# Performance work log

Hardware: AMD Instinct MI355X
Metric: run time of the kernel (lower is better)

## Reference

```python
import jax, jax.numpy as jnp
import numpy as np

GH, GW = 8, 8  # hypernetwork patch grid
EPS = 1e-5


def image_coords(b, h, w, dtype):
    # matches get_image_coordinates: channel0 = x (varies along W), channel1 = y (varies along H)
    xs = jnp.linspace(-1.0, 1.0, w, dtype=dtype)
    ys = jnp.linspace(-1.0, 1.0, h, dtype=dtype)
    X = jnp.broadcast_to(xs[None, :], (h, w))
    Y = jnp.broadcast_to(ys[:, None], (h, w))
    g = jnp.stack([X, Y], axis=0)  # [2,H,W]
    return jnp.broadcast_to(g[None], (b, 2, h, w))


def im2col3(x):
    # reflect-pad 3x3 im2col -> [B,C,9,H,W]
    H, W = x.shape[2], x.shape[3]
    xp = jnp.pad(x, ((0, 0), (0, 0), (1, 1), (1, 1)), mode='reflect')
    cols = [xp[:, :, i:i + H, j:j + W] for i in range(3) for j in range(3)]
    return jnp.stack(cols, axis=2)


def meta_dw3(x, wsig):
    # depthwise 3x3 conv with per-patch weights. wsig: [B, C*9, GH, GW]
    B, C, H, W = x.shape
    p, q = H // GH, W // GW
    cols = im2col3(x).reshape(B, C, 9, GH, p, GW, q)
    Wd = wsig.reshape(B, C, 9, GH, GW)
    out = jnp.einsum('bctuivj,bctuv->bcuivj', cols, Wd)
    return out.reshape(B, C, H, W)


def meta_pw(x, wsig, out_nc):
    # pointwise 1x1 conv with per-patch weights. wsig: [B, out_nc*C, GH, GW]
    B, C, H, W = x.shape
    p, q = H // GH, W // GW
    xr = x.reshape(B, C, GH, p, GW, q)
    Wp = wsig.reshape(B, out_nc, C, GH, GW)
    out = jnp.einsum('bcuivj,bocuv->bouivj', xr, Wp)
    return out.reshape(B, out_nc, H, W)


def batch_norm(x, g, b):
    m = jnp.mean(x, (0, 2, 3), keepdims=True)
    v = jnp.var(x, (0, 2, 3), keepdims=True)
    return (x - m) * jax.lax.rsqrt(v + EPS) * g[None, :, None, None] + b[None, :, None, None]


def relu6(x):
    return jnp.clip(x, 0.0, 6.0)


def hpir(x, wsig, out_nc, g_dw, b_dw, g_pw, b_pw):
    # HyperPatchInvertedResidual, expand_ratio=1, stride=1, in_nc != out_nc -> no residual
    C = x.shape[1]
    n_dw = C * 9
    h = relu6(batch_norm(meta_dw3(x, wsig[:, :n_dw]), g_dw, b_dw))
    h = batch_norm(meta_pw(h, wsig[:, n_dw:n_dw + out_nc * C], out_nc), g_pw, b_pw)
    return h


def resize_bilinear(p, hw):
    B, C = p.shape[0], p.shape[1]
    return jax.image.resize(p, (B, C, hw[0], hw[1]), method='bilinear')


def decoder_forward(x_img, f0, f1, w0, w1, w2,
                    g_dw0, b_dw0, g_pw0, b_pw0,
                    g_dw1, b_dw1, g_pw1, b_pw1,
                    g_dw2, b_dw2, g_pw2, b_pw2):
    feats = [x_img, f0, f1]  # [img] + features[:-1]
    level_w = [w0, w1, w2]
    level_out = [64, 32, 21]
    bn_p = [(g_dw0, b_dw0, g_pw0, b_pw0),
            (g_dw1, b_dw1, g_pw1, b_pw1),
            (g_dw2, b_dw2, g_pw2, b_pw2)]
    p = None
    for level in range(3):
        f = feats[-level - 1]
        if p is None:
            p = f
        else:
            if p.shape[2:] != f.shape[2:]:
                p = resize_bilinear(p, f.shape[2:])
            p = jnp.concatenate([f, p], axis=1)
        B, _, H, W = p.shape
        p = jnp.concatenate([image_coords(B, H, W, p.dtype), p], axis=1)
        g_dw, b_dw, g_pw, b_pw = bn_p[level]
        p = hpir(p, level_w[level], level_out[level], g_dw, b_dw, g_pw, b_pw)
    return p


def setup_inputs() -> dict:
    key = jax.random.key(0)
    ks = jax.random.split(key, 8)
    inp = {
        'x_img': jax.random.normal(ks[0], (4, 3, 256, 256), jnp.float32),
        'f0': jax.random.normal(ks[1], (4, 32, 64, 64), jnp.float32),
        'f1': jax.random.normal(ks[2], (4, 64, 32, 32), jnp.float32),
        'w0': jax.random.normal(ks[3], (4, 4818, 8, 8), jnp.float32) * 0.1,
        'w1': jax.random.normal(ks[4], (4, 4018, 8, 8), jnp.float32) * 0.1,
        'w2': jax.random.normal(ks[5], (4, 1110, 8, 8), jnp.float32) * 0.1,
    }
    for name, c in [('dw0', 66), ('pw0', 64), ('dw1', 98), ('pw1', 32), ('dw2', 37), ('pw2', 21)]:
        inp['g_' + name] = jnp.ones((c,), jnp.float32)
        inp['b_' + name] = jnp.zeros((c,), jnp.float32)
    return inp


def reference(x_img, f0, f1, w0, w1, w2,
              g_dw0, b_dw0, g_pw0, b_pw0,
              g_dw1, b_dw1, g_pw1, b_pw1,
              g_dw2, b_dw2, g_pw2, b_pw2):
    return decoder_forward(x_img, f0, f1, w0, w1, w2,
                           g_dw0, b_dw0, g_pw0, b_pw0,
                           g_dw1, b_dw1, g_pw1, b_pw1,
                           g_dw2, b_dw2, g_pw2, b_pw2)
```

## Files before the change

### kernel.cpp

```cpp
#include <hip/hip_runtime.h>

#define EPS 1e-5f

__device__ __forceinline__ int reflect_idx(int i, int n) {
    if (i < 0) return -i;
    if (i >= n) return 2 * n - 2 - i;
    return i;
}

__device__ __forceinline__ float bilin(const float* __restrict__ pb, int Hp, float sy, float sx) {
    int y0 = (int)floorf(sy), x0 = (int)floorf(sx);
    float fy = sy - y0, fx = sx - x0;
    int y0c = min(max(y0, 0), Hp - 1), y1c = min(max(y0 + 1, 0), Hp - 1);
    int x0c = min(max(x0, 0), Hp - 1), x1c = min(max(x0 + 1, 0), Hp - 1);
    float v00 = pb[y0c * Hp + x0c], v01 = pb[y0c * Hp + x1c];
    float v10 = pb[y1c * Hp + x0c], v11 = pb[y1c * Hp + x1c];
    return v00 * (1 - fy) * (1 - fx) + v01 * (1 - fy) * fx
         + v10 * fy * (1 - fx) + v11 * fy * fx;
}

__device__ __forceinline__ void reduce_ss_lds(const float* __restrict__ part,
                                              const float* __restrict__ g,
                                              const float* __restrict__ bb,
                                              float* ss, int C, float invN, int tid) {
    for (int c = tid; c < C; c += 256) {
        float s1 = 0.f, s2 = 0.f;
#pragma unroll 8
        for (int s = 0; s < 64; ++s) {
            s1 += part[s * 2 * C + 2 * c];
            s2 += part[s * 2 * C + 2 * c + 1];
        }
        float m = s1 * invN;
        float var = s2 * invN - m * m;
        float sc = g[c] * rsqrtf(var + EPS);
        ss[2 * c] = sc;
        ss[2 * c + 1] = bb[c] - m * sc;
    }
}

template <int LEVEL, bool WRITE>
__global__ __launch_bounds__(256)
void fused_dw_kernel(const float* __restrict__ feat, const float* __restrict__ prev,
                     const float* __restrict__ part_prev, const float* __restrict__ g_prev,
                     const float* __restrict__ b_prev, float invN_prev,
                     const float* __restrict__ wsig,
                     float* __restrict__ out, float* __restrict__ part) {
    constexpr int C    = LEVEL == 0 ? 66 : LEVEL == 1 ? 98 : 37;
    constexpr int H    = LEVEL == 0 ? 32 : LEVEL == 1 ? 64 : 256;
    constexpr int TILE = LEVEL == 2 ? 32 : 16;
    constexpr int NT   = H / TILE;
    constexpr int PXPT = (TILE * TILE) / 256;
    constexpr int WC   = LEVEL == 0 ? 4818 : LEVEL == 1 ? 4018 : 1110;
    constexpr int NF   = LEVEL == 0 ? 64 : LEVEL == 1 ? 32 : 3;
    constexpr int Hp   = LEVEL == 1 ? 32 : 64;
    constexpr int Cp   = LEVEL == 1 ? 64 : 32;
    constexpr int P    = H / 8;
    constexpr float SC = LEVEL == 1 ? 0.5f : 0.25f;
    constexpr int HS   = TILE + 2;
    constexpr int PSS  = (LEVEL == 0) ? 2 : 2 * Cp;

    __shared__ float sh[HS * HS];
    __shared__ float pssl[PSS];
    int tid = threadIdx.x, bid = blockIdx.x;
    int tile = bid % (NT * NT);
    int c = (bid / (NT * NT)) % C;
    int b = bid / (NT * NT * C);
    int ty0 = (tile / NT) * TILE, tx0 = (tile % NT) * TILE;

    if constexpr (LEVEL != 0) {
        reduce_ss_lds(part_prev, g_prev, b_prev, pssl, Cp, invN_prev, tid);
        __syncthreads();
    }

    for (int i = tid; i < HS * HS; i += 256) {
        int h = reflect_idx(ty0 - 1 + i / HS, H);
        int w = reflect_idx(tx0 - 1 + i % HS, H);
        float val;
        if (c == 0)      val = -1.f + 2.f * w / (H - 1);
        else if (c == 1) val = -1.f + 2.f * h / (H - 1);
        else if (c < 2 + NF) val = feat[((size_t)(b * NF + c - 2) * H + h) * H + w];
        else {
            int o = c - 2 - NF;
            const float* pb = prev + (size_t)(b * Cp + o) * Hp * Hp;
            float raw = bilin(pb, Hp, (h + 0.5f) * SC - 0.5f, (w + 0.5f) * SC - 0.5f);
            val = raw * pssl[2 * o] + pssl[2 * o + 1];
        }
        sh[i] = val;
    }
    __syncthreads();

    float s1 = 0.f, s2 = 0.f;
    float* ob = out + (((size_t)(b * C + c)) * H + ty0) * H + tx0;
    float wreg[9];
    if constexpr (TILE == P) {
        const float* wb = wsig + ((size_t)(b * WC + c * 9)) * 64 + (ty0 / P) * 8 + (tx0 / P);
#pragma unroll
        for (int t = 0; t < 9; ++t) wreg[t] = wb[(size_t)t * 64];
    }
#pragma unroll
    for (int k = 0; k < PXPT; ++k) {
        int px = tid + k * 256;
        int tyy = px / TILE, txx = px % TILE;
        if constexpr (TILE != P) {
            int u = (ty0 + tyy) / P, vv = (tx0 + txx) / P;
            const float* wb = wsig + ((size_t)(b * WC + c * 9)) * 64 + u * 8 + vv;
#pragma unroll
            for (int t = 0; t < 9; ++t) wreg[t] = wb[(size_t)t * 64];
        }
        float acc = 0.f;
#pragma unroll
        for (int t = 0; t < 9; ++t)
            acc += wreg[t] * sh[(tyy + t / 3) * HS + txx + t % 3];
        if constexpr (WRITE) ob[tyy * H + txx] = acc;
        s1 += acc; s2 += acc * acc;
    }
#pragma unroll
    for (int off = 32; off; off >>= 1) {
        s1 += __shfl_xor(s1, off);
        s2 += __shfl_xor(s2, off);
    }
    __shared__ float r1[4], r2[4];
    int wave = tid >> 6;
    if ((tid & 63) == 0) { r1[wave] = s1; r2[wave] = s2; }
    __syncthreads();
    if (tid == 0) {
        int slot = bid & 63;
        atomicAdd(&part[slot * 2 * C + 2 * c],     r1[0] + r1[1] + r1[2] + r1[3]);
        atomicAdd(&part[slot * 2 * C + 2 * c + 1], r2[0] + r2[1] + r2[2] + r2[3]);
    }
}

__global__ __launch_bounds__(256)
void dw2_col_kernel(const float* __restrict__ ximg, const float* __restrict__ prev,
                    const float* __restrict__ part_prev, const float* __restrict__ g_prev,
                    const float* __restrict__ b_prev,
                    const float* __restrict__ wsig,
                    float* __restrict__ out, float* __restrict__ part) {
    const int C = 37, H = 256, W = 256, WC = 1110, Hp = 64, Cp = 32;
    const int S = 260;
    __shared__ float sh[10 * S];
    __shared__ float pssl[64];
    __shared__ float lwv[72];
    __shared__ float r1[4], r2[4];

    int tid = threadIdx.x, bid = blockIdx.x;
    int rb = bid & 31;
    int c  = (bid >> 5) % C;
    int b  = bid / (32 * C);
    int ty0 = rb * 8;
    int u = rb >> 2;

    reduce_ss_lds(part_prev, g_prev, b_prev, pssl, Cp, 1.f / 16384.f, tid);
    if (tid < 72) {
        int v = tid / 9, t = tid % 9;
        lwv[tid] = wsig[((size_t)(b * WC + c * 9 + t)) * 64 + u * 8 + v];
    }
    __syncthreads();

    for (int i = tid; i < 10 * 258; i += 256) {
        int r = i / 258, wcol = i % 258 - 1;
        int h = reflect_idx(ty0 - 1 + r, H);
        int w = reflect_idx(wcol, W);
        float val;
        if (c == 0)      val = -1.f + 2.f * w / 255.f;
        else if (c == 1) val = -1.f + 2.f * h / 255.f;
        else if (c < 5)  val = ximg[((size_t)(b * 3 + c - 2) * H + h) * W + w];
        else {
            int o = c - 5;
            const float* pb = prev + (size_t)(b * Cp + o) * Hp * Hp;
            float raw = bilin(pb, Hp, (h + 0.5f) * 0.25f - 0.5f, (w + 0.5f) * 0.25f - 0.5f);
            val = raw * pssl[2 * o] + pssl[2 * o + 1];
        }
        sh[r * S + wcol + 1] = val;
    }
    __syncthreads();

    int t = tid;
    int v = t >> 5;
    float wr[9];
#pragma unroll
    for (int tap = 0; tap < 9; ++tap) wr[tap] = lwv[v * 9 + tap];

    float px[8];
#pragma unroll
    for (int k = 0; k < 8; ++k) px[k] = 0.f;

#pragma unroll
    for (int r = 0; r < 10; ++r) {
        float L = sh[r * S + t];
        float M = sh[r * S + t + 1];
        float R = sh[r * S + t + 2];
#pragma unroll
        for (int dr = 0; dr < 3; ++dr) {
            int k = r - dr;
            if (k >= 0 && k < 8)
                px[k] += wr[dr * 3] * L + wr[dr * 3 + 1] * M + wr[dr * 3 + 2] * R;
        }
    }

    float* ob = out + (((size_t)(b * C + c)) * H + ty0) * W + t;
    float s1 = 0.f, s2 = 0.f;
#pragma unroll
    for (int k = 0; k < 8; ++k) {
        ob[k * W] = px[k];
        s1 += px[k]; s2 += px[k] * px[k];
    }
#pragma unroll
    for (int off = 32; off; off >>= 1) {
        s1 += __shfl_xor(s1, off);
        s2 += __shfl_xor(s2, off);
    }
    int wave = tid >> 6;
    if ((tid & 63) == 0) { r1[wave] = s1; r2[wave] = s2; }
    __syncthreads();
    if (tid == 0) {
        int slot = bid & 63;
        atomicAdd(&part[slot * 2 * C + 2 * c],     r1[0] + r1[1] + r1[2] + r1[3]);
        atomicAdd(&part[slot * 2 * C + 2 * c + 1], r2[0] + r2[1] + r2[2] + r2[3]);
    }
}

template <int C, int ONC, int H, int PX_T, int OC_T>
__global__ __launch_bounds__(256)
void pw_small_kernel(const float* __restrict__ x, const float* __restrict__ wsig,
                     const float* __restrict__ part_in, const float* __restrict__ g,
                     const float* __restrict__ bb, float invN,
                     float* __restrict__ out, float* __restrict__ part, int WC, int ndw) {
    constexpr int P = H / 8;
    constexpr int OC_I = ONC / OC_T;
    __shared__ float lw[ONC * C];
    __shared__ float lx[C * PX_T];
    __shared__ float ssl[2 * C];
    int tid = threadIdx.x, bid = blockIdx.x;
    int uv = bid & 63, b = bid >> 6;
    int u = uv >> 3, v = uv & 7;

    const size_t wbase = ((size_t)b * WC + ndw) * 64 + uv;
    for (int i = tid; i < ONC * C; i += 256) lw[i] = wsig[wbase + (size_t)i * 64];
    reduce_ss_lds(part_in, g, bb, ssl, C, invN, tid);
    __syncthreads();

    for (int i = tid; i < C * PX_T; i += 256) {
        int c = i / PX_T, pxl = i % PX_T;
        int h = u * P + pxl / P, w = v * P + pxl % P;
        float xv = x[(((size_t)b * C + c) * H + h) * H + w];
        lx[i] = fminf(fmaxf(xv * ssl[2 * c] + ssl[2 * c + 1], 0.f), 6.f);
    }
    __syncthreads();

    int px_id = tid % PX_T, oc_id = tid / PX_T;
    int h = u * P + px_id / P, w = v * P + px_id % P;
    float acc[OC_I];
#pragma unroll
    for (int oi = 0; oi < OC_I; ++oi) acc[oi] = 0.f;
    for (int c = 0; c < C; ++c) {
        float xv = lx[c * PX_T + px_id];
#pragma unroll
        for (int oi = 0; oi < OC_I; ++oi)
            acc[oi] += lw[(oc_id * OC_I + oi) * C + c] * xv;
    }
    float* ob = out + (((size_t)b * ONC) * H + h) * H + w;
#pragma unroll
    for (int oi = 0; oi < OC_I; ++oi)
        ob[(size_t)(oc_id * OC_I + oi) * H * H] = acc[oi];

    constexpr int GROUP = (PX_T < 64) ? PX_T : 64;
    int lane = tid & 63;
    int slot = bid & 63;
#pragma unroll
    for (int oi = 0; oi < OC_I; ++oi) {
        float s1 = acc[oi], s2 = acc[oi] * acc[oi];
#pragma unroll
        for (int off = GROUP / 2; off; off >>= 1) {
            s1 += __shfl_xor(s1, off);
            s2 += __shfl_xor(s2, off);
        }
        if ((lane & (GROUP - 1)) == 0) {
            int o = oc_id * OC_I + oi;
            atomicAdd(&part[slot * 2 * ONC + 2 * o], s1);
            atomicAdd(&part[slot * 2 * ONC + 2 * o + 1], s2);
        }
    }
}

__global__ __launch_bounds__(256)
void pw2_kernel(const float* __restrict__ x, const float* __restrict__ wsig,
                const float* __restrict__ part_in, const float* __restrict__ g,
                const float* __restrict__ bb,
                float* __restrict__ out, float* __restrict__ part) {
    const int C = 37, ONC = 21, H = 256, PATCH = 32, WC = 1110, NDW = 333;
    __shared__ float lw[ONC * C];
    __shared__ float ssl[2 * C];
    __shared__ float r1[4][ONC], r2[4][ONC];
    int tid = threadIdx.x, bid = blockIdx.x;
    int uv = bid & 63, b = bid >> 6;
    int y0 = (uv >> 3) * PATCH, x0 = (uv & 7) * PATCH;

    for (int i = tid; i < ONC * C; i += 256) lw[i] = wsig[((size_t)(b * WC + NDW) + i) * 64 + uv];
    reduce_ss_lds(part_in, g, bb, ssl, C, 1.f / 262144.f, tid);
    __syncthreads();

    int row = tid >> 3, col = (tid & 7) * 4;
    const float* xb = x + (((size_t)b * C) * H + y0 + row) * H + x0 + col;
    float4 acc[ONC];
#pragma unroll
    for (int o = 0; o < ONC; ++o) acc[o] = make_float4(0.f, 0.f, 0.f, 0.f);

    for (int c = 0; c < C; ++c) {
        float4 xv = *(const float4*)(xb + (size_t)c * H * H);
        float sc = ssl[2 * c], sb = ssl[2 * c + 1];
        xv.x = fminf(fmaxf(xv.x * sc + sb, 0.f), 6.f);
        xv.y = fminf(fmaxf(xv.y * sc + sb, 0.f), 6.f);
        xv.z = fminf(fmaxf(xv.z * sc + sb, 0.f), 6.f);
        xv.w = fminf(fmaxf(xv.w * sc + sb, 0.f), 6.f);
#pragma unroll
        for (int o = 0; o < ONC; ++o) {
            float wv = lw[o * C + c];
            acc[o].x += wv * xv.x;
            acc[o].y += wv * xv.y;
            acc[o].z += wv * xv.z;
            acc[o].w += wv * xv.w;
        }
    }
    float* ob = out + (((size_t)b * ONC) * H + y0 + row) * H + x0 + col;
#pragma unroll
    for (int o = 0; o < ONC; ++o) *(float4*)(ob + (size_t)o * H * H) = acc[o];

    int wave = tid >> 6, lane = tid & 63;
#pragma unroll
    for (int o = 0; o < ONC; ++o) {
        float s1 = acc[o].x + acc[o].y + acc[o].z + acc[o].w;
        float s2 = acc[o].x * acc[o].x + acc[o].y * acc[o].y
                 + acc[o].z * acc[o].z + acc[o].w * acc[o].w;
#pragma unroll
        for (int off = 32; off; off >>= 1) {
            s1 += __shfl_xor(s1, off);
            s2 += __shfl_xor(s2, off);
        }
        if (lane == 0) { r1[wave][o] = s1; r2[wave][o] = s2; }
    }
    __syncthreads();
    int slot = bid & 63;
    for (int o = tid; o < ONC; o += 256) {
        atomicAdd(&part[slot * 42 + 2 * o],     r1[0][o] + r1[1][o] + r1[2][o] + r1[3][o]);
        atomicAdd(&part[slot * 42 + 2 * o + 1], r2[0][o] + r2[1][o] + r2[2][o] + r2[3][o]);
    }
}

__global__ __launch_bounds__(256)
void finalbn_kernel(float* __restrict__ out, const float* __restrict__ part_in,
                    const float* __restrict__ g, const float* __restrict__ bb) {
    __shared__ float ssl[42];
    reduce_ss_lds(part_in, g, bb, ssl, 21, 1.f / 262144.f, threadIdx.x);
    __syncthreads();
    const int total4 = 4 * 21 * 256 * 256 / 4;
    for (int idx = blockIdx.x * 256 + threadIdx.x; idx < total4; idx += gridDim.x * 256) {
        int c = (idx / (256 * 256 / 4)) % 21;
        float4 v = ((float4*)out)[idx];
        float sc = ssl[2 * c], sb = ssl[2 * c + 1];
        v.x = v.x * sc + sb; v.y = v.y * sc + sb; v.z = v.z * sc + sb; v.w = v.w * sc + sb;
        ((float4*)out)[idx] = v;
    }
}

extern "C" void kernel_launch(void* const* d_in, const int* in_sizes, int n_in,
                              void* d_out, int out_size, void* d_ws, size_t ws_size,
                              hipStream_t stream) {
    const float* x_img = (const float*)d_in[0];
    const float* f0    = (const float*)d_in[1];
    const float* f1    = (const float*)d_in[2];
    const float* w0    = (const float*)d_in[3];
    const float* w1    = (const float*)d_in[4];
    const float* w2    = (const float*)d_in[5];
    const float* g_dw0 = (const float*)d_in[6],  *b_dw0 = (const float*)d_in[7];
    const float* g_pw0 = (const float*)d_in[8],  *b_pw0 = (const float*)d_in[9];
    const float* g_dw1 = (const float*)d_in[10], *b_dw1 = (const float*)d_in[11];
    const float* g_pw1 = (const float*)d_in[12], *b_pw1 = (const float*)d_in[13];
    const float* g_dw2 = (const float*)d_in[14], *b_dw2 = (const float*)d_in[15];
    const float* g_pw2 = (const float*)d_in[16], *b_pw2 = (const float*)d_in[17];
    float* out = (float*)d_out;
    float* ws = (float*)d_ws;

    float* part_dw0 = ws;
    float* part_pw0 = ws + 8448;
    float* part_dw1 = ws + 16640;
    float* part_pw1 = ws + 29184;
    float* part_dw2 = ws + 33280;
    float* part_pw2 = ws + 38016;
    float* pw0raw = ws + 40704;
    float* pw1raw = pw0raw + 262144;
    float* bigA   = pw1raw + 524288;

    hipMemsetAsync(ws, 0, 40704 * sizeof(float), stream);

    fused_dw_kernel<0, true><<<4 * 66 * 4, 256, 0, stream>>>(
        f1, nullptr, nullptr, nullptr, nullptr, 0.f, w0, bigA, part_dw0);
    pw_small_kernel<66, 64, 32, 16, 16><<<256, 256, 0, stream>>>(
        bigA, w0, part_dw0, g_dw0, b_dw0, 1.f / 4096.f, pw0raw, part_pw0, 4818, 594);
    fused_dw_kernel<1, true><<<4 * 98 * 16, 256, 0, stream>>>(
        f0, pw0raw, part_pw0, g_pw0, b_pw0, 1.f / 4096.f, w1, bigA, part_dw1);
    pw_small_kernel<98, 32, 64, 64, 4><<<256, 256, 0, stream>>>(
        bigA, w1, part_dw1, g_dw1, b_dw1, 1.f / 16384.f, pw1raw, part_pw1, 4018, 882);
    dw2_col_kernel<<<4 * 37 * 32, 256, 0, stream>>>(
        x_img, pw1raw, part_pw1, g_pw1, b_pw1, w2, bigA, part_dw2);
    pw2_kernel<<<256, 256, 0, stream>>>(bigA, w2, part_dw2, g_dw2, b_dw2, out, part_pw2);
    finalbn_kernel<<<1024, 256, 0, stream>>>(out, part_pw2, g_pw2, b_pw2);
}
```

Measured before the change: 147.5 us.

## Parallelize BN stat reduction, transpose w2, split pw2 into more blocks

Replaces the serial per-channel 64-slot BN partial reduction with a grouped two-stage reduction that spreads slots across all threads. Adds a pre-pass that transposes the level-2 hypernetwork weights so dw2 and pw2 read them contiguously. Restructures dw2 halo loading so each thread handles one column with hoisted horizontal bilinear terms. pw2 is split into 4x more blocks with scalar per-pixel accumulation, trading float4 loads for more parallelism. The cost is an extra kernel launch and extra workspace.

```diff
diff --git a/kernel.cpp b/kernel.cpp
--- a/kernel.cpp
+++ b/kernel.cpp
@@ -19,23 +19,47 @@
          + v10 * fy * (1 - fx) + v11 * fy * fx;
 }
 
-__device__ __forceinline__ void reduce_ss_lds(const float* __restrict__ part,
-                                              const float* __restrict__ g,
-                                              const float* __restrict__ bb,
-                                              float* ss, int C, float invN, int tid) {
-    for (int c = tid; c < C; c += 256) {
+template <int C>
+__device__ __forceinline__ void reduce_ss_wide(const float* __restrict__ part,
+                                               const float* __restrict__ g,
+                                               const float* __restrict__ bb,
+                                               float* ss, float* scratch,
+                                               float invN, int tid) {
+    constexpr int G = 256 / C;
+    int grp = tid / C;
+    int c = tid - grp * C;
+    if (grp < G) {
         float s1 = 0.f, s2 = 0.f;
-#pragma unroll 8
-        for (int s = 0; s < 64; ++s) {
+        for (int s = grp; s < 64; s += G) {
             s1 += part[s * 2 * C + 2 * c];
             s2 += part[s * 2 * C + 2 * c + 1];
         }
+        scratch[grp * 2 * C + 2 * c] = s1;
+        scratch[grp * 2 * C + 2 * c + 1] = s2;
+    }
+    __syncthreads();
+    if (tid < C) {
+        float s1 = 0.f, s2 = 0.f;
+#pragma unroll
+        for (int gg = 0; gg < G; ++gg) {
+            s1 += scratch[gg * 2 * C + 2 * tid];
+            s2 += scratch[gg * 2 * C + 2 * tid + 1];
+        }
         float m = s1 * invN;
         float var = s2 * invN - m * m;
-        float sc = g[c] * rsqrtf(var + EPS);
-        ss[2 * c] = sc;
-        ss[2 * c + 1] = bb[c] - m * sc;
-    }
+        float sc = g[tid] * rsqrtf(var + EPS);
+        ss[2 * tid] = sc;
+        ss[2 * tid + 1] = bb[tid] - m * sc;
+    }
+    __syncthreads();
+}
+
+__global__ __launch_bounds__(256)
+void wtrans_kernel(const float* __restrict__ w2, float* __restrict__ wT) {
+    int uv = blockIdx.x & 63, b = blockIdx.x >> 6;
+    const float* src = w2 + (size_t)b * 1110 * 64 + uv;
+    float* dst = wT + ((size_t)(b * 64 + uv)) * 1110;
+    for (int i = threadIdx.x; i < 1110; i += 256) dst[i] = src[(size_t)i * 64];
 }
 
 template <int LEVEL, bool WRITE>
@@ -45,22 +69,23 @@
                      const float* __restrict__ b_prev, float invN_prev,
                      const float* __restrict__ wsig,
                      float* __restrict__ out, float* __restrict__ part) {
-    constexpr int C    = LEVEL == 0 ? 66 : LEVEL == 1 ? 98 : 37;
-    constexpr int H    = LEVEL == 0 ? 32 : LEVEL == 1 ? 64 : 256;
-    constexpr int TILE = LEVEL == 2 ? 32 : 16;
+    constexpr int C    = LEVEL == 0 ? 66 : 98;
+    constexpr int H    = LEVEL == 0 ? 32 : 64;
+    constexpr int TILE = 16;
     constexpr int NT   = H / TILE;
     constexpr int PXPT = (TILE * TILE) / 256;
-    constexpr int WC   = LEVEL == 0 ? 4818 : LEVEL == 1 ? 4018 : 1110;
-    constexpr int NF   = LEVEL == 0 ? 64 : LEVEL == 1 ? 32 : 3;
+    constexpr int WC   = LEVEL == 0 ? 4818 : 4018;
+    constexpr int NF   = LEVEL == 0 ? 64 : 32;
     constexpr int Hp   = LEVEL == 1 ? 32 : 64;
     constexpr int Cp   = LEVEL == 1 ? 64 : 32;
     constexpr int P    = H / 8;
-    constexpr float SC = LEVEL == 1 ? 0.5f : 0.25f;
+    constexpr float SC = 0.5f;
     constexpr int HS   = TILE + 2;
     constexpr int PSS  = (LEVEL == 0) ? 2 : 2 * Cp;
 
     __shared__ float sh[HS * HS];
     __shared__ float pssl[PSS];
+    __shared__ float scratch[512];
     int tid = threadIdx.x, bid = blockIdx.x;
     int tile = bid % (NT * NT);
     int c = (bid / (NT * NT)) % C;
@@ -68,8 +93,7 @@
     int ty0 = (tile / NT) * TILE, tx0 = (tile % NT) * TILE;
 
     if constexpr (LEVEL != 0) {
-        reduce_ss_lds(part_prev, g_prev, b_prev, pssl, Cp, invN_prev, tid);
-        __syncthreads();
+        reduce_ss_wide<Cp>(part_prev, g_prev, b_prev, pssl, scratch, invN_prev, tid);
     }
 
     for (int i = tid; i < HS * HS; i += 256) {
@@ -134,13 +158,14 @@
 void dw2_col_kernel(const float* __restrict__ ximg, const float* __restrict__ prev,
                     const float* __restrict__ part_prev, const float* __restrict__ g_prev,
                     const float* __restrict__ b_prev,
-                    const float* __restrict__ wsig,
+                    const float* __restrict__ wT,
                     float* __restrict__ out, float* __restrict__ part) {
-    const int C = 37, H = 256, W = 256, WC = 1110, Hp = 64, Cp = 32;
+    const int C = 37, H = 256, W = 256, Hp = 64, Cp = 32;
     const int S = 260;
     __shared__ float sh[10 * S];
     __shared__ float pssl[64];
     __shared__ float lwv[72];
+    __shared__ float scratch[512];
     __shared__ float r1[4], r2[4];
 
     int tid = threadIdx.x, bid = blockIdx.x;
@@ -150,28 +175,64 @@
     int ty0 = rb * 8;
     int u = rb >> 2;
 
-    reduce_ss_lds(part_prev, g_prev, b_prev, pssl, Cp, 1.f / 16384.f, tid);
     if (tid < 72) {
-        int v = tid / 9, t = tid % 9;
-        lwv[tid] = wsig[((size_t)(b * WC + c * 9 + t)) * 64 + u * 8 + v];
-    }
-    __syncthreads();
-
-    for (int i = tid; i < 10 * 258; i += 256) {
-        int r = i / 258, wcol = i % 258 - 1;
+        int v = tid / 9, t = tid - v * 9;
+        lwv[tid] = wT[((size_t)(b * 64 + u * 8 + v)) * 1110 + c * 9 + t];
+    }
+    reduce_ss_wide<32>(part_prev, g_prev, b_prev, pssl, scratch, 1.f / 16384.f, tid);
+
+    const float* pb = (c >= 5) ? prev + (size_t)(b * Cp + (c - 5)) * Hp * Hp : nullptr;
+    const float* xrow = (c >= 2 && c < 5) ? ximg + (size_t)(b * 3 + c - 2) * H * W : nullptr;
+    float cx = -1.f + tid * (2.f / 255.f);
+    float sxm = (tid + 0.5f) * 0.25f - 0.5f;
+    int x0m = (int)floorf(sxm);
+    float fxm = sxm - x0m;
+    int x0cm = min(max(x0m, 0), Hp - 1), x1cm = min(max(x0m + 1, 0), Hp - 1);
+
+#pragma unroll
+    for (int r = 0; r < 10; ++r) {
         int h = reflect_idx(ty0 - 1 + r, H);
-        int w = reflect_idx(wcol, W);
         float val;
-        if (c == 0)      val = -1.f + 2.f * w / 255.f;
-        else if (c == 1) val = -1.f + 2.f * h / 255.f;
-        else if (c < 5)  val = ximg[((size_t)(b * 3 + c - 2) * H + h) * W + w];
+        if (c == 0)      val = cx;
+        else if (c == 1) val = -1.f + h * (2.f / 255.f);
+        else if (c < 5)  val = xrow[h * W + tid];
         else {
-            int o = c - 5;
-            const float* pb = prev + (size_t)(b * Cp + o) * Hp * Hp;
-            float raw = bilin(pb, Hp, (h + 0.5f) * 0.25f - 0.5f, (w + 0.5f) * 0.25f - 0.5f);
-            val = raw * pssl[2 * o] + pssl[2 * o + 1];
-        }
-        sh[r * S + wcol + 1] = val;
+            float sy = (h + 0.5f) * 0.25f - 0.5f;
+            int y0 = (int)floorf(sy);
+            float fy = sy - y0;
+            int y0c = min(max(y0, 0), Hp - 1), y1c = min(max(y0 + 1, 0), Hp - 1);
+            const float* q0 = pb + y0c * Hp;
+            const float* q1 = pb + y1c * Hp;
+            float a0 = q0[x0cm] + (q0[x1cm] - q0[x0cm]) * fxm;
+            float a1 = q1[x0cm] + (q1[x1cm] - q1[x0cm]) * fxm;
+            float raw = a0 + (a1 - a0) * fy;
+            val = raw * pssl[2 * (c - 5)] + pssl[2 * (c - 5) + 1];
+        }
+        sh[r * S + tid + 1] = val;
+    }
+    if (tid < 20) {
+        int r = tid >> 1, side = tid & 1;
+        int wimg = side ? 254 : 1;
+        int h = reflect_idx(ty0 - 1 + r, H);
+        float val;
+        if (c == 0)      val = -1.f + wimg * (2.f / 255.f);
+        else if (c == 1) val = -1.f + h * (2.f / 255.f);
+        else if (c < 5)  val = xrow[h * W + wimg];
+        else {
+            float sx = (wimg + 0.5f) * 0.25f - 0.5f;
+            int x0 = (int)floorf(sx); float fx = sx - x0;
+            int x0c = min(max(x0, 0), Hp - 1), x1c = min(max(x0 + 1, 0), Hp - 1);
+            float sy = (h + 0.5f) * 0.25f - 0.5f;
+            int y0 = (int)floorf(sy); float fy = sy - y0;
+            int y0c = min(max(y0, 0), Hp - 1), y1c = min(max(y0 + 1, 0), Hp - 1);
+            const float* q0 = pb + y0c * Hp;
+            const float* q1 = pb + y1c * Hp;
+            float a0 = q0[x0c] + (q0[x1c] - q0[x0c]) * fx;
+            float a1 = q1[x0c] + (q1[x1c] - q1[x0c]) * fx;
+            float raw = a0 + (a1 - a0) * fy;
+            val = raw * pssl[2 * (c - 5)] + pssl[2 * (c - 5) + 1];
+        }
+        sh[r * S + (side ? 257 : 0)] = val;
     }
     __syncthreads();
 
@@ -231,14 +292,14 @@
     __shared__ float lw[ONC * C];
     __shared__ float lx[C * PX_T];
     __shared__ float ssl[2 * C];
+    __shared__ float scratch[512];
     int tid = threadIdx.x, bid = blockIdx.x;
     int uv = bid & 63, b = bid >> 6;
     int u = uv >> 3, v = uv & 7;
 
     const size_t wbase = ((size_t)b * WC + ndw) * 64 + uv;
     for (int i = tid; i < ONC * C; i += 256) lw[i] = wsig[wbase + (size_t)i * 64];
-    reduce_ss_lds(part_in, g, bb, ssl, C, invN, tid);
-    __syncthreads();
+    reduce_ss_wide<C>(part_in, g, bb, ssl, scratch, invN, tid);
 
     for (int i = tid; i < C * PX_T; i += 256) {
         int c = i / PX_T, pxl = i % PX_T;
@@ -284,54 +345,46 @@
 }
 
 __global__ __launch_bounds__(256)
-void pw2_kernel(const float* __restrict__ x, const float* __restrict__ wsig,
+void pw2_kernel(const float* __restrict__ x, const float* __restrict__ wT,
                 const float* __restrict__ part_in, const float* __restrict__ g,
                 const float* __restrict__ bb,
                 float* __restrict__ out, float* __restrict__ part) {
-    const int C = 37, ONC = 21, H = 256, PATCH = 32, WC = 1110, NDW = 333;
-    __shared__ float lw[ONC * C];
-    __shared__ float ssl[2 * C];
+    const int C = 37, ONC = 21, H = 256;
+    __shared__ float lw[777];
+    __shared__ float ssl[74];
+    __shared__ float scratch[512];
     __shared__ float r1[4][ONC], r2[4][ONC];
     int tid = threadIdx.x, bid = blockIdx.x;
-    int uv = bid & 63, b = bid >> 6;
-    int y0 = (uv >> 3) * PATCH, x0 = (uv & 7) * PATCH;
-
-    for (int i = tid; i < ONC * C; i += 256) lw[i] = wsig[((size_t)(b * WC + NDW) + i) * 64 + uv];
-    reduce_ss_lds(part_in, g, bb, ssl, C, 1.f / 262144.f, tid);
-    __syncthreads();
-
-    int row = tid >> 3, col = (tid & 7) * 4;
-    const float* xb = x + (((size_t)b * C) * H + y0 + row) * H + x0 + col;
-    float4 acc[ONC];
-#pragma unroll
-    for (int o = 0; o < ONC; ++o) acc[o] = make_float4(0.f, 0.f, 0.f, 0.f);
+    int chunk = bid & 3;
+    int uv = (bid >> 2) & 63;
+    int b = bid >> 8;
+    int y0 = (uv >> 3) * 32 + chunk * 8, x0 = (uv & 7) * 32;
+
+    const float* wt = wT + ((size_t)(b * 64 + uv)) * 1110 + 333;
+    for (int i = tid; i < 777; i += 256) lw[i] = wt[i];
+    reduce_ss_wide<37>(part_in, g, bb, ssl, scratch, 1.f / 262144.f, tid);
+
+    int row = tid >> 5, col = tid & 31;
+    const float* xb = x + (((size_t)(b * C)) * H + y0 + row) * H + x0 + col;
+    float acc[ONC];
+#pragma unroll
+    for (int o = 0; o < ONC; ++o) acc[o] = 0.f;
 
     for (int c = 0; c < C; ++c) {
-        float4 xv = *(const float4*)(xb + (size_t)c * H * H);
-        float sc = ssl[2 * c], sb = ssl[2 * c + 1];
-        xv.x = fminf(fmaxf(xv.x * sc + sb, 0.f), 6.f);
-        xv.y = fminf(fmaxf(xv.y * sc + sb, 0.f), 6.f);
-        xv.z = fminf(fmaxf(xv.z * sc + sb, 0.f), 6.f);
-        xv.w = fminf(fmaxf(xv.w * sc + sb, 0.f), 6.f);
-#pragma unroll
-        for (int o = 0; o < ONC; ++o) {
-            float wv = lw[o * C + c];
-            acc[o].x += wv * xv.x;
-            acc[o].y += wv * xv.y;
-            acc[o].z += wv * xv.z;
-            acc[o].w += wv * xv.w;
-        }
-    }
-    float* ob = out + (((size_t)b * ONC) * H + y0 + row) * H + x0 + col;
-#pragma unroll
-    for (int o = 0; o < ONC; ++o) *(float4*)(ob + (size_t)o * H * H) = acc[o];
+        float xv = xb[(size_t)c * H * H];
+        xv = fminf(fmaxf(xv * ssl[2 * c] + ssl[2 * c + 1], 0.f), 6.f);
+#pragma unroll
+        for (int o = 0; o < ONC; ++o)
+            acc[o] += lw[o * C + c] * xv;
+    }
+    float* ob = out + (((size_t)(b * ONC)) * H + y0 + row) * H + x0 + col;
+#pragma unroll
+    for (int o = 0; o < ONC; ++o) ob[(size_t)o * H * H] = acc[o];
 
     int wave = tid >> 6, lane = tid & 63;
 #pragma unroll
     for (int o = 0; o < ONC; ++o) {
-        float s1 = acc[o].x + acc[o].y + acc[o].z + acc[o].w;
-        float s2 = acc[o].x * acc[o].x + acc[o].y * acc[o].y
-                 + acc[o].z * acc[o].z + acc[o].w * acc[o].w;
+        float s1 = acc[o], s2 = acc[o] * acc[o];
 #pragma unroll
         for (int off = 32; off; off >>= 1) {
             s1 += __shfl_xor(s1, off);
@@ -351,8 +404,8 @@
 void finalbn_kernel(float* __restrict__ out, const float* __restrict__ part_in,
                     const float* __restrict__ g, const float* __restrict__ bb) {
     __shared__ float ssl[42];
-    reduce_ss_lds(part_in, g, bb, ssl, 21, 1.f / 262144.f, threadIdx.x);
-    __syncthreads();
+    __shared__ float scratch[512];
+    reduce_ss_wide<21>(part_in, g, bb, ssl, scratch, 1.f / 262144.f, threadIdx.x);
     const int total4 = 4 * 21 * 256 * 256 / 4;
     for (int idx = blockIdx.x * 256 + threadIdx.x; idx < total4; idx += gridDim.x * 256) {
         int c = (idx / (256 * 256 / 4)) % 21;
@@ -387,11 +440,13 @@
     float* part_pw1 = ws + 29184;
     float* part_dw2 = ws + 33280;
     float* part_pw2 = ws + 38016;
-    float* pw0raw = ws + 40704;
+    float* wT     = ws + 40704;
+    float* pw0raw = ws + 324864;
     float* pw1raw = pw0raw + 262144;
     float* bigA   = pw1raw + 524288;
 
     hipMemsetAsync(ws, 0, 40704 * sizeof(float), stream);
+    wtrans_kernel<<<256, 256, 0, stream>>>(w2, wT);
 
     fused_dw_kernel<0, true><<<4 * 66 * 4, 256, 0, stream>>>(
         f1, nullptr, nullptr, nullptr, nullptr, 0.f, w0, bigA, part_dw0);
@@ -402,7 +457,7 @@
     pw_small_kernel<98, 32, 64, 64, 4><<<256, 256, 0, stream>>>(
         bigA, w1, part_dw1, g_dw1, b_dw1, 1.f / 16384.f, pw1raw, part_pw1, 4018, 882);
     dw2_col_kernel<<<4 * 37 * 32, 256, 0, stream>>>(
-        x_img, pw1raw, part_pw1, g_pw1, b_pw1, w2, bigA, part_dw2);
-    pw2_kernel<<<256, 256, 0, stream>>>(bigA, w2, part_dw2, g_dw2, b_dw2, out, part_pw2);
+        x_img, pw1raw, part_pw1, g_pw1, b_pw1, wT, bigA, part_dw2);
+    pw2_kernel<<<1024, 256, 0, stream>>>(bigA, wT, part_dw2, g_dw2, b_dw2, out, part_pw2);
     finalbn_kernel<<<1024, 256, 0, stream>>>(out, part_pw2, g_pw2, b_pw2);
 }
```

New measurement: 157.8 us. 7.0% more time.
